# Performance work log

Hardware: AMD Instinct MI355X
Metric: run time of the kernel (lower is better)

Reference implementation:

```python
import jax, jax.numpy as jnp
import numpy as np

B, T, D, H = 2, 1024, 1024, 16
WINDOW = 32
KSZ = 2 * WINDOW + 1
MAXG = 32


def setup_inputs() -> dict:
    key = jax.random.key(0)
    ks = jax.random.split(key, 5)
    s = 0.02
    x = jax.random.normal(ks[0], (B, T, D), jnp.float32)
    Wq = jax.random.normal(ks[1], (D, D), jnp.float32) * s
    Wk = jax.random.normal(ks[2], (D, D), jnp.float32) * s
    Wv = jax.random.normal(ks[3], (D, D), jnp.float32) * s
    Wo = jax.random.normal(ks[4], (D, D), jnp.float32) * s
    # global tokens: one every T//MAXG positions (same for every batch row)
    global_mask = jnp.tile((jnp.arange(T) % (T // MAXG) == 0)[None, :], (B, 1))
    return {"x": x, "global_mask": global_mask, "Wq": Wq, "Wk": Wk,
            "Wv": Wv, "Wo": Wo, "maxG": MAXG}


def reference(x, global_mask, Wq, Wk, Wv, Wo, maxG):
    Bb, Tt, Dm = x.shape
    dh = Dm // H
    scale = dh ** -0.5

    def proj(W):
        return (x @ W.T).reshape(Bb, Tt, H, dh).transpose(0, 2, 1, 3)  # (B,H,T,dh)

    q, k, v = proj(Wq), proj(Wk), proj(Wv)

    # sliding windows via zero-padded gather (== F.unfold with padding=WINDOW)
    widx = jnp.arange(Tt)[:, None] + jnp.arange(KSZ)[None, :]  # index into padded axis

    def windows(t):
        tp = jnp.pad(t, ((0, 0), (0, 0), (WINDOW, WINDOW), (0, 0)))
        return tp[:, :, widx, :]  # (B,H,T,KSZ,dh)

    Kw, Vw = windows(k), windows(v)
    scores_local = jnp.einsum('bhtd,bhtwd->bhtw', q, Kw) * scale

    # pack global-token indices (stable argsort puts True positions first, in order)
    order = jnp.argsort(jnp.logical_not(global_mask), axis=1, stable=True)
    gidx = order[:, :maxG]                                   # (B,maxG)
    gvalid = jnp.take_along_axis(global_mask, gidx, axis=1)  # (B,maxG) bool
    gather_b = jax.vmap(lambda arr, i: arr[:, i, :])         # (H,T,dh),(maxG,)->(H,maxG,dh)
    Kg = gather_b(k, gidx) * gvalid[:, None, :, None]
    Vg = gather_b(v, gidx) * gvalid[:, None, :, None]

    scores_global = jnp.einsum('bhtd,bhgd->bhtg', q, Kg) * scale
    scores_global = jnp.where(gvalid[:, None, None, :], scores_global, -1e9)

    attn = jax.nn.softmax(jnp.concatenate([scores_local, scores_global], axis=-1), axis=-1)
    wl, wg = attn[..., :KSZ], attn[..., KSZ:]
    ctx = (jnp.einsum('bhtw,bhtwd->bhtd', wl, Vw)
           + jnp.einsum('bhtg,bhgd->bhtd', wg, Vg))
    out = ctx.transpose(0, 2, 1, 3).reshape(Bb, Tt, Dm) @ Wo.T

    # ---- debug full attention map (vectorized replica of the per-token loop) ----
    t = jnp.arange(Tt)
    left = jnp.maximum(0, t - WINDOW)
    win_len = jnp.minimum(Tt, t + WINDOW + 1) - left           # (T,)
    valid_w = jnp.arange(KSZ)[None, :] < win_len[:, None]      # (T,KSZ)
    s_loc = jnp.where(valid_w[None, None], scores_local, -jnp.inf)
    attn_d = jax.nn.softmax(jnp.concatenate([s_loc, scores_global], axis=-1), axis=-1)
    wl_d = attn_d[..., :KSZ] * valid_w[None, None]             # (B,H,T,KSZ)
    wg_d = attn_d[..., KSZ:] * gvalid[:, None, None, :]        # (B,H,T,maxG)
    cols = jnp.minimum(left[:, None] + jnp.arange(KSZ)[None, :], Tt - 1)  # (T,KSZ)
    rows = jnp.broadcast_to(t[:, None], (Tt, KSZ))
    full_attn = jnp.zeros((Bb, H, Tt, Tt), x.dtype)
    full_attn = full_attn.at[:, :, rows, cols].add(wl_d)
    full_attn = jax.vmap(lambda fa, w, gi: fa.at[:, :, gi].add(w))(full_attn, wg_d, gidx)
    return out, full_attn
```

## Files before the change

kernel.cpp:

```cpp
#include <hip/hip_runtime.h>

#define T_   1024
#define B_   2
#define H_   16
#define DH   64
#define D_   1024
#define WND  32
#define KSZ  65
#define NG   32

typedef float f32x4 __attribute__((ext_vector_type(4)));
typedef __bf16 bf16x8 __attribute__((ext_vector_type(8)));
typedef __bf16 bf16x4 __attribute__((ext_vector_type(4)));
typedef unsigned short u16x4 __attribute__((ext_vector_type(4)));

__device__ __forceinline__ unsigned short f2bf(float f) {
  unsigned u = __float_as_uint(f);
  return (unsigned short)((u + 0x7fffu + ((u >> 16) & 1u)) >> 16);
}

template<bool F32>
__device__ __forceinline__ bf16x8 load_cvt8(const char* p) {
  if constexpr (F32) {
    f32x4 a = *(const f32x4*)p;
    f32x4 b = *(const f32x4*)(p + 16);
    bf16x8 r;
    r[0] = (__bf16)a[0]; r[1] = (__bf16)a[1]; r[2] = (__bf16)a[2]; r[3] = (__bf16)a[3];
    r[4] = (__bf16)b[0]; r[5] = (__bf16)b[1]; r[6] = (__bf16)b[2]; r[7] = (__bf16)b[3];
    return r;
  } else {
    return *(const bf16x8*)p;
  }
}

template<int MODE, int BM, bool AF32, bool BF32>
__global__ __launch_bounds__(256) void gemm128(
    const void* __restrict__ A,
    const void* __restrict__ B0, const void* __restrict__ B1, const void* __restrict__ B2,
    void* __restrict__ C0v, void* __restrict__ C1v, void* __restrict__ C2v,
    const int* __restrict__ mask, int* __restrict__ gidxo, float* __restrict__ gvalo) {
  constexpr int K = 1024;
  constexpr int FM = BM / 32;
  constexpr int ACH = BM * 8 / 256;
  constexpr int WM = BM / 2;
  constexpr int AE = AF32 ? 4 : 2, BE = BF32 ? 4 : 2;

  if (MODE == 0 && blockIdx.x == 16) {
    if (blockIdx.y == 0 && blockIdx.z == 0 && threadIdx.x < 128) {
      int b = threadIdx.x >> 6, lane = threadIdx.x & 63;
      const int* mb = mask + b * T_;
      unsigned long long lanemask = (1ull << lane) - 1ull;
      int base = 0;
      for (int c = 0; c < 16 && base < NG; ++c) {
        int t = c * 64 + lane;
        bool m = mb[t] != 0;
        unsigned long long bal = __ballot(m);
        int rank = __popcll(bal & lanemask);
        if (m && base + rank < NG) { gidxo[b*NG+base+rank] = t; gvalo[b*NG+base+rank] = 1.f; }
        base += __popcll(bal);
      }
      if (base < NG) {
        for (int c = 0; c < 16 && base < NG; ++c) {
          int t = c * 64 + lane;
          bool m = mb[t] == 0;
          unsigned long long bal = __ballot(m);
          int rank = __popcll(bal & lanemask);
          if (m && base + rank < NG) { gidxo[b*NG+base+rank] = t; gvalo[b*NG+base+rank] = 0.f; }
          base += __popcll(bal);
        }
      }
    }
    return;
  }

  __shared__ __attribute__((aligned(16))) unsigned short SMEM[BM * 64 + 128 * 64];
  unsigned short* As = SMEM;
  unsigned short* Bs = SMEM + BM * 64;

  int m0 = blockIdx.x * BM, n0 = blockIdx.y * 128;
  int zz = (MODE == 0) ? blockIdx.z : 0;
  const char* Ab = (const char*)A;
  const char* Bb = (const char*)((MODE == 0) ? (zz == 0 ? B0 : (zz == 1 ? B1 : B2)) : B0);

  int tid = threadIdx.x;
  int w = tid >> 6, l = tid & 63;
  int wr = w >> 1, wc = w & 1;
  int lr = l & 15, kg = l >> 4;

  f32x4 acc[FM][4] = {};

  for (int kt = 0; kt < K; kt += 64) {
    __syncthreads();
#pragma unroll
    for (int i = 0; i < ACH; ++i) {
      int ci = tid + 256 * i;
      int row = ci >> 3, c8 = ci & 7;
      *(bf16x8*)&As[row * 64 + ((c8 ^ (row & 7)) * 8)] =
          load_cvt8<AF32>(Ab + ((size_t)(m0 + row) * K + kt + c8 * 8) * AE);
    }
#pragma unroll
    for (int i = 0; i < 4; ++i) {
      int ci = tid + 256 * i;
      int row = ci >> 3, c8 = ci & 7;
      *(bf16x8*)&Bs[row * 64 + ((c8 ^ (row & 7)) * 8)] =
          load_cvt8<BF32>(Bb + ((size_t)(n0 + row) * K + kt + c8 * 8) * BE);
    }
    __syncthreads();
#pragma unroll
    for (int kk = 0; kk < 2; ++kk) {
      int c8 = kk * 4 + kg;
      bf16x8 af[FM], bfr[4];
#pragma unroll
      for (int mi = 0; mi < FM; ++mi) {
        int row = wr * WM + mi * 16 + lr;
        af[mi] = *(bf16x8*)&As[row * 64 + ((c8 ^ (row & 7)) * 8)];
      }
#pragma unroll
      for (int ni = 0; ni < 4; ++ni) {
        int row = wc * 64 + ni * 16 + lr;
        bfr[ni] = *(bf16x8*)&Bs[row * 64 + ((c8 ^ (row & 7)) * 8)];
      }
#pragma unroll
      for (int mi = 0; mi < FM; ++mi)
#pragma unroll
        for (int ni = 0; ni < 4; ++ni)
          acc[mi][ni] = __builtin_amdgcn_mfma_f32_16x16x32_bf16(af[mi], bfr[ni], acc[mi][ni], 0, 0, 0);
    }
  }

  if (MODE == 1) {
    float* C = (float*)C0v;
#pragma unroll
    for (int mi = 0; mi < FM; ++mi)
#pragma unroll
      for (int ni = 0; ni < 4; ++ni) {
        int mbase = m0 + wr * WM + mi * 16 + (l >> 4) * 4;
        int n = n0 + wc * 64 + ni * 16 + lr;
#pragma unroll
        for (int r = 0; r < 4; ++r)
          C[(size_t)(mbase + r) * 1024 + n] = acc[mi][ni][r];
      }
  } else if (zz < 2) {
    unsigned short* C = (unsigned short*)(zz == 0 ? C0v : C1v);
#pragma unroll
    for (int mi = 0; mi < FM; ++mi)
#pragma unroll
      for (int ni = 0; ni < 4; ++ni) {
        int mbase = m0 + wr * WM + mi * 16 + (l >> 4) * 4;
        int n = n0 + wc * 64 + ni * 16 + lr;
#pragma unroll
        for (int r = 0; r < 4; ++r) {
          __bf16 v = (__bf16)acc[mi][ni][r];
          C[(size_t)(mbase + r) * 1024 + n] = *(unsigned short*)&v;
        }
      }
  } else {
    __syncthreads();
    char* Tb = (char*)SMEM;
#pragma unroll
    for (int mi = 0; mi < FM; ++mi)
#pragma unroll
      for (int ni = 0; ni < 4; ++ni) {
        int mb2 = wr * WM + mi * 16 + (l >> 4) * 4;
        int nl = wc * 64 + ni * 16 + lr;
        bf16x4 pk;
        pk[0] = (__bf16)acc[mi][ni][0]; pk[1] = (__bf16)acc[mi][ni][1];
        pk[2] = (__bf16)acc[mi][ni][2]; pk[3] = (__bf16)acc[mi][ni][3];
        *(bf16x4*)(Tb + ((nl * 256 + mb2 * 2) ^ ((nl & 7) << 4))) = pk;
      }
    __syncthreads();
    unsigned short* C = (unsigned short*)C2v;
    int bb = m0 >> 10, tbase = m0 & 1023;
#pragma unroll
    for (int it = 0; it < 8; ++it) {
      int ci = tid + 256 * it;
      int dl = ci >> 4, tc = ci & 15;
      bf16x8 v = *(bf16x8*)(Tb + ((dl * 256 + tc * 16) ^ ((dl & 7) << 4)));
      int n = n0 + dl, hh = n >> 6, dd = n & 63;
      *(bf16x8*)&C[((size_t)(bb * H_ + hh) * DH + dd) * T_ + tbase + tc * 8] = v;
    }
  }
}

__global__ __launch_bounds__(512, 4) void attn_kernel(
    const unsigned short* __restrict__ qg, const unsigned short* __restrict__ kg_,
    const unsigned short* __restrict__ vg,
    const int* __restrict__ gidx_g, const float* __restrict__ gval_g,
    unsigned short* __restrict__ ctxb, float* __restrict__ fa) {
  int tid = threadIdx.x;
  int t0 = blockIdx.x * 32;
  int h = blockIdx.y, b = blockIdx.z;
  int lane = tid & 63, wv = tid >> 6;

  __shared__ __attribute__((aligned(16))) unsigned short QbL[32 * 64];
  __shared__ __attribute__((aligned(16))) unsigned short KbL[128 * 64];
  __shared__ __attribute__((aligned(16))) unsigned short VtL[64 * 128];
  __shared__ __attribute__((aligned(16))) unsigned short WbL[32 * 128];
  __shared__ __attribute__((aligned(16))) float Sf[32][132];
  __shared__ float m_out_s[32], invdo_s[32], rowfac_s[32];
  __shared__ int   gidx_s[32];
  __shared__ float gval_s[32];

  if (tid < 32) { gidx_s[tid] = gidx_g[b * NG + tid]; gval_s[tid] = gval_g[b * NG + tid]; }
  ((unsigned long long*)WbL)[tid] = 0ull;
  ((unsigned long long*)WbL)[tid + 512] = 0ull;
  __syncthreads();

  const unsigned short* qbh = qg + (size_t)(b * T_ + t0) * D_ + h * DH;
  const unsigned short* kbh = kg_ + (size_t)(b * T_) * D_ + h * DH;
  const unsigned short* vbh = vg + (size_t)(b * H_ + h) * DH * T_;

  if (tid < 256) {
    int r = tid >> 3, c8 = tid & 7;
    bf16x8 v = *(const bf16x8*)(qbh + (size_t)r * D_ + c8 * 8);
    *(bf16x8*)((char*)QbL + ((r * 128 + c8 * 16) ^ ((r & 7) << 4))) = v;
  }
#pragma unroll
  for (int it = 0; it < 2; ++it) {
    int fi = tid + it * 512;
    int r = fi >> 3, c8 = fi & 7;
    int col; bool valid;
    if (r < 96) { col = t0 - 32 + r; valid = (col >= 0 && col < T_); }
    else { int g = r - 96; valid = gval_s[g] > 0.f; col = valid ? gidx_s[g] : 0; }
    bf16x8 v = {};
    if (valid) v = *(const bf16x8*)(kbh + (size_t)col * D_ + c8 * 8);
    *(bf16x8*)((char*)KbL + ((r * 128 + c8 * 16) ^ ((r & 7) << 4))) = v;
  }
#pragma unroll
  for (int it = 0; it < 2; ++it) {
    int fi = tid + it * 512;
    if (fi < 768) {
      int d = fi / 12, rc = fi % 12;
      int cb = t0 - 32 + rc * 8;
      bf16x8 v = {};
      if (cb >= 0 && cb < T_) v = *(const bf16x8*)(vbh + d * T_ + cb);
      *(bf16x8*)((char*)VtL + ((d * 256 + rc * 16) ^ ((d & 7) << 4))) = v;
    }
  }
#pragma unroll
  for (int it = 0; it < 4; ++it) {
    int fi = tid + it * 512;
    int d = fi >> 5, g = fi & 31;
    unsigned short v = 0;
    if (gval_s[g] > 0.f) v = vbh[d * T_ + gidx_s[g]];
    *(unsigned short*)((char*)VtL + ((d * 256 + (96 + g) * 2) ^ ((d & 7) << 4))) = v;
  }
  __syncthreads();

  {
    int mt = wv & 1, nq = wv >> 1;
    int lrr = lane & 15, kgl = lane >> 4;
    int arow = mt * 16 + lrr;
    f32x4 acc0 = {}, acc1 = {};
#pragma unroll
    for (int s = 0; s < 2; ++s) {
      int c = s * 4 + kgl;
      bf16x8 a = *(bf16x8*)((char*)QbL + ((arow * 128 + c * 16) ^ ((arow & 7) << 4)));
      int br0 = nq * 32 + lrr, br1 = nq * 32 + 16 + lrr;
      bf16x8 b0 = *(bf16x8*)((char*)KbL + ((br0 * 128 + c * 16) ^ ((br0 & 7) << 4)));
      bf16x8 b1 = *(bf16x8*)((char*)KbL + ((br1 * 128 + c * 16) ^ ((br1 & 7) << 4)));
      acc0 = __builtin_amdgcn_mfma_f32_16x16x32_bf16(a, b0, acc0, 0, 0, 0);
      acc1 = __builtin_amdgcn_mfma_f32_16x16x32_bf16(a, b1, acc1, 0, 0, 0);
    }
    int orow = mt * 16 + (lane >> 4) * 4;
#pragma unroll
    for (int i = 0; i < 4; ++i) {
      Sf[orow + i][nq * 32 + lrr] = acc0[i] * 0.125f;
      Sf[orow + i][nq * 32 + 16 + lrr] = acc1[i] * 0.125f;
    }
  }
  __syncthreads();

  {
    int r = tid >> 4, lg = tid & 15;
    int t_abs = t0 + r;
    int left = (t_abs - WND > 0) ? (t_abs - WND) : 0;
    int tmp = t_abs + WND + 1; if (tmp > T_) tmp = T_;
    int wl = tmp - left;
    float sv[8]; bool vld[8], vdd[8];
#pragma unroll
    for (int ii = 0; ii < 8; ++ii) {
      int c = lg + ii * 16;
      bool loc = (c >= r && c <= r + 64);
      bool glob = (c >= 96);
      float s = Sf[r][c];
      if (glob && !(gval_s[c - 96] > 0.f)) s = -1e9f;
      vld[ii] = loc || glob;
      vdd[ii] = loc ? ((c - r) < wl) : glob;
      sv[ii] = s;
    }
    float mo = -1e30f, md = -1e30f;
#pragma unroll
    for (int ii = 0; ii < 8; ++ii) {
      if (vld[ii]) mo = fmaxf(mo, sv[ii]);
      if (vdd[ii]) md = fmaxf(md, sv[ii]);
    }
#pragma unroll
    for (int o = 1; o < 16; o <<= 1) {
      mo = fmaxf(mo, __shfl_xor(mo, o, 16));
      md = fmaxf(md, __shfl_xor(md, o, 16));
    }
    float eo = 0.f, ed = 0.f;
#pragma unroll
    for (int ii = 0; ii < 8; ++ii) {
      if (vld[ii]) eo += __expf(sv[ii] - mo);
      if (vdd[ii]) ed += __expf(sv[ii] - md);
    }
#pragma unroll
    for (int o = 1; o < 16; o <<= 1) {
      eo += __shfl_xor(eo, o, 16);
      ed += __shfl_xor(ed, o, 16);
    }
    if (lg == 0) {
      m_out_s[r] = mo;
      invdo_s[r] = 1.f / eo;
      rowfac_s[r] = (eo / ed) * __expf(mo - md);
    }
  }
  __syncthreads();

  for (int idx = tid; idx < 32 * 97; idx += 512) {
    int t = idx / 97;
    int j = idx - t * 97;
    int cc = (j < KSZ) ? (t + j) : (j + 31);
    float s = Sf[t][cc];
    float wgt = __expf(s - m_out_s[t]) * invdo_s[t];
    Sf[t][cc] = wgt;
    *(unsigned short*)((char*)WbL + ((t * 256 + cc * 2) ^ ((t & 7) << 4))) = f2bf(wgt);
  }
  __syncthreads();

  {
    int mt = wv >> 1, nt = wv & 1;
    int lrr = lane & 15, kgl = lane >> 4;
    int arow = mt * 16 + lrr;
    int brow = nt * 16 + lrr;
    f32x4 acc = {};
#pragma unroll
    for (int s = 0; s < 4; ++s) {
      int c = s * 4 + kgl;
      bf16x8 a = *(bf16x8*)((char*)VtL + ((arow * 256 + c * 16) ^ ((arow & 7) << 4)));
      bf16x8 bb = *(bf16x8*)((char*)WbL + ((brow * 256 + c * 16) ^ ((brow & 7) << 4)));
      acc = __builtin_amdgcn_mfma_f32_16x16x32_bf16(a, bb, acc, 0, 0, 0);
    }
    int t = nt * 16 + lrr;
    int dbase = mt * 16 + (lane >> 4) * 4;
    u16x4 st;
    st.x = f2bf(acc[0]); st.y = f2bf(acc[1]); st.z = f2bf(acc[2]); st.w = f2bf(acc[3]);
    *(u16x4*)(ctxb + ((size_t)(b * T_ + t0 + t)) * D_ + h * DH + dbase) = st;
  }

  {
    int rp = tid >> 8;
    int c0 = (tid & 255) * 4;
    unsigned gm = 0;
#pragma unroll
    for (int g = 0; g < NG; ++g) {
      int gc = gidx_s[g];
      if (gval_s[g] > 0.f && gc >= c0 && gc < c0 + 4) gm |= (1u << g);
    }
#pragma unroll 2
    for (int rr = 0; rr < 16; ++rr) {
      int r = rr * 2 + rp;
      int t_abs = t0 + r;
      int left = (t_abs - WND > 0) ? (t_abs - WND) : 0;
      int tmp = t_abs + WND + 1; if (tmp > T_) tmp = T_;
      int wl = tmp - left;
      float rf = rowfac_s[r];
      f32x4 o = {0.f, 0.f, 0.f, 0.f};
      int jj0 = c0 - left;
      if (jj0 > -4 && jj0 < wl) {
#pragma unroll
        for (int e = 0; e < 4; ++e) {
          int jj = jj0 + e;
          if (jj >= 0 && jj < wl) o[e] = Sf[r][r + jj] * rf;
        }
      }
      if (gm) {
        unsigned mm = gm;
        while (mm) {
          int g = __ffs(mm) - 1; mm &= mm - 1;
          int e = gidx_s[g] - c0;
          o[e] += Sf[r][96 + g] * rf;
        }
      }
      float* dst = fa + (((size_t)(b * H_ + h) * T_) + t_abs) * T_ + c0;
      *(f32x4*)dst = o;
    }
  }
}

extern "C" void kernel_launch(void* const* d_in, const int* in_sizes, int n_in,
                              void* d_out, int out_size, void* d_ws, size_t ws_size,
                              hipStream_t stream) {
  const float* x   = (const float*)d_in[0];
  const int* gmask = (const int*)d_in[1];
  const float* wq  = (const float*)d_in[2];
  const float* wk  = (const float*)d_in[3];
  const float* wv  = (const float*)d_in[4];
  const float* wo  = (const float*)d_in[5];

  char* ws = (char*)d_ws;
  unsigned short* qb   = (unsigned short*)ws;
  unsigned short* kb   = qb + 2 * 1048576;
  unsigned short* vtb  = kb + 2 * 1048576;
  unsigned short* ctxb = vtb + 2 * 1048576;
  int*   gidx = (int*)(ctxb + 2 * 1048576);
  float* gval = (float*)(gidx + 64);

  float* outp = (float*)d_out;
  float* fa   = outp + 2097152;

  gemm128<0, 128, true, true><<<dim3(17, 8, 3), dim3(256), 0, stream>>>(
      x, wq, wk, wv, qb, kb, vtb, gmask, gidx, gval);
  attn_kernel<<<dim3(32, 16, 2), dim3(512), 0, stream>>>(qb, kb, vtb, gidx, gval, ctxb, fa);
  gemm128<1, 64, false, true><<<dim3(32, 8, 1), dim3(256), 0, stream>>>(
      ctxb, wo, wo, wo, outp, outp, outp, nullptr, nullptr, nullptr);
}
```

Baseline: 95.02 us.

## Precast inputs to bf16, use global_load_lds, move full_attn write into output GEMM

A separate conversion kernel casts x and all four weight matrices to bf16 once per call. The GEMMs can then stream tiles into LDS with direct global_load_lds. The dense full_attn map write moves out of the attention kernel. Attention now spills its weights and row factors to a workspace, and extra blocks in the output-projection GEMM scatter the 128MB map concurrently with the matmul tiles. This aims to overlap the bandwidth-bound map write with GEMM compute, at the cost of an extra conversion pass and a roughly 16MB workspace round trip.

```diff
diff --git a/kernel.cpp b/kernel.cpp
--- a/kernel.cpp
+++ b/kernel.cpp
@@ -19,34 +19,19 @@
   return (unsigned short)((u + 0x7fffu + ((u >> 16) & 1u)) >> 16);
 }
 
-template<bool F32>
-__device__ __forceinline__ bf16x8 load_cvt8(const char* p) {
-  if constexpr (F32) {
-    f32x4 a = *(const f32x4*)p;
-    f32x4 b = *(const f32x4*)(p + 16);
-    bf16x8 r;
-    r[0] = (__bf16)a[0]; r[1] = (__bf16)a[1]; r[2] = (__bf16)a[2]; r[3] = (__bf16)a[3];
-    r[4] = (__bf16)b[0]; r[5] = (__bf16)b[1]; r[6] = (__bf16)b[2]; r[7] = (__bf16)b[3];
-    return r;
-  } else {
-    return *(const bf16x8*)p;
-  }
-}
-
-template<int MODE, int BM, bool AF32, bool BF32>
-__global__ __launch_bounds__(256) void gemm128(
-    const void* __restrict__ A,
-    const void* __restrict__ B0, const void* __restrict__ B1, const void* __restrict__ B2,
-    void* __restrict__ C0v, void* __restrict__ C1v, void* __restrict__ C2v,
+__device__ __forceinline__ void gload16(const unsigned short* g, unsigned short* l) {
+  __builtin_amdgcn_global_load_lds(
+      (const __attribute__((address_space(1))) unsigned int*)g,
+      (__attribute__((address_space(3))) unsigned int*)l, 16, 0, 0);
+}
+
+__global__ __launch_bounds__(256) void cvt_kernel(const float* __restrict__ x,
+    const float* __restrict__ wq, const float* __restrict__ wk,
+    const float* __restrict__ wv, const float* __restrict__ wo,
+    unsigned short* __restrict__ dst,
     const int* __restrict__ mask, int* __restrict__ gidxo, float* __restrict__ gvalo) {
-  constexpr int K = 1024;
-  constexpr int FM = BM / 32;
-  constexpr int ACH = BM * 8 / 256;
-  constexpr int WM = BM / 2;
-  constexpr int AE = AF32 ? 4 : 2, BE = BF32 ? 4 : 2;
-
-  if (MODE == 0 && blockIdx.x == 16) {
-    if (blockIdx.y == 0 && blockIdx.z == 0 && threadIdx.x < 128) {
+  if (blockIdx.x == 6144) {
+    if (threadIdx.x < 128) {
       int b = threadIdx.x >> 6, lane = threadIdx.x & 63;
       const int* mb = mask + b * T_;
       unsigned long long lanemask = (1ull << lane) - 1ull;
@@ -72,17 +57,102 @@
     }
     return;
   }
-
+  int idx = (blockIdx.x * 256 + threadIdx.x) * 4;
+  int r = idx >> 20;
+  const float* src; int off;
+  if (r < 2)       { src = x;  off = idx; }
+  else if (r == 2) { src = wq; off = idx - 2 * 1048576; }
+  else if (r == 3) { src = wk; off = idx - 3 * 1048576; }
+  else if (r == 4) { src = wv; off = idx - 4 * 1048576; }
+  else             { src = wo; off = idx - 5 * 1048576; }
+  f32x4 v = *(const f32x4*)(src + off);
+  u16x4 o;
+  o.x = f2bf(v[0]); o.y = f2bf(v[1]); o.z = f2bf(v[2]); o.w = f2bf(v[3]);
+  *(u16x4*)(dst + idx) = o;
+}
+
+template<int MODE, int BM>
+__global__ __launch_bounds__(256) void gemm128(
+    const unsigned short* __restrict__ A,
+    const unsigned short* __restrict__ B0, const unsigned short* __restrict__ B1,
+    const unsigned short* __restrict__ B2,
+    void* __restrict__ C0v, void* __restrict__ C1v, void* __restrict__ C2v,
+    const float* __restrict__ wsum, const float* __restrict__ rfb,
+    const int* __restrict__ gidxg, const float* __restrict__ gvalg,
+    float* __restrict__ fa) {
+  constexpr int K = 1024;
+  constexpr int FM = BM / 32;
+  constexpr int ACH = BM * 8 / 256;
+  constexpr int WM = BM / 2;
   __shared__ __attribute__((aligned(16))) unsigned short SMEM[BM * 64 + 128 * 64];
+  int tid = threadIdx.x;
+
+  if (MODE == 1 && blockIdx.x >= 32) {
+    int wid = (blockIdx.x - 32) * 8 + blockIdx.y;
+    float* Ws = (float*)SMEM;
+    float* rfs = Ws + 32 * 128;
+    int* gidxs = (int*)(rfs + 32);
+    float* gvals = (float*)(gidxs + 32);
+#pragma unroll 1
+    for (int u = 0; u < 4; ++u) {
+      int unit = wid * 4 + u;
+      int b = unit >> 9, bh = unit >> 5;
+      int t0 = (unit & 31) * 32;
+      __syncthreads();
+      const float* src = wsum + (size_t)unit * 4096;
+      *(f32x4*)&Ws[tid * 4]        = *(const f32x4*)&src[tid * 4];
+      *(f32x4*)&Ws[1024 + tid * 4] = *(const f32x4*)&src[1024 + tid * 4];
+      *(f32x4*)&Ws[2048 + tid * 4] = *(const f32x4*)&src[2048 + tid * 4];
+      *(f32x4*)&Ws[3072 + tid * 4] = *(const f32x4*)&src[3072 + tid * 4];
+      if (tid < 32) {
+        rfs[tid] = rfb[unit * 32 + tid];
+        gidxs[tid] = gidxg[b * NG + tid];
+        gvals[tid] = gvalg[b * NG + tid];
+      }
+      __syncthreads();
+      int c0 = tid * 4;
+      unsigned gm = 0;
+#pragma unroll
+      for (int g = 0; g < NG; ++g) {
+        int gc = gidxs[g];
+        if (gvals[g] > 0.f && gc >= c0 && gc < c0 + 4) gm |= (1u << g);
+      }
+#pragma unroll 2
+      for (int r = 0; r < 32; ++r) {
+        int t_abs = t0 + r;
+        int left = (t_abs - WND > 0) ? (t_abs - WND) : 0;
+        int tmp = t_abs + WND + 1; if (tmp > T_) tmp = T_;
+        int wl = tmp - left;
+        float rf = rfs[r];
+        f32x4 o = {0.f, 0.f, 0.f, 0.f};
+        int jj0 = c0 - left;
+        if (jj0 > -4 && jj0 < wl) {
+#pragma unroll
+          for (int e = 0; e < 4; ++e) {
+            int jj = jj0 + e;
+            if (jj >= 0 && jj < wl) o[e] = Ws[r * 128 + r + jj] * rf;
+          }
+        }
+        if (gm) {
+          unsigned mm = gm;
+          while (mm) {
+            int g = __ffs(mm) - 1; mm &= mm - 1;
+            o[gidxs[g] - c0] += Ws[r * 128 + 96 + g] * rf;
+          }
+        }
+        *(f32x4*)(fa + ((size_t)(bh * T_) + t_abs) * T_ + c0) = o;
+      }
+    }
+    return;
+  }
+
   unsigned short* As = SMEM;
   unsigned short* Bs = SMEM + BM * 64;
-
   int m0 = blockIdx.x * BM, n0 = blockIdx.y * 128;
   int zz = (MODE == 0) ? blockIdx.z : 0;
-  const char* Ab = (const char*)A;
-  const char* Bb = (const char*)((MODE == 0) ? (zz == 0 ? B0 : (zz == 1 ? B1 : B2)) : B0);
-
-  int tid = threadIdx.x;
+  const unsigned short* Ab = A;
+  const unsigned short* Bb = (MODE == 0) ? (zz == 0 ? B0 : (zz == 1 ? B1 : B2)) : B0;
+
   int w = tid >> 6, l = tid & 63;
   int wr = w >> 1, wc = w & 1;
   int lr = l & 15, kg = l >> 4;
@@ -94,16 +164,14 @@
 #pragma unroll
     for (int i = 0; i < ACH; ++i) {
       int ci = tid + 256 * i;
-      int row = ci >> 3, c8 = ci & 7;
-      *(bf16x8*)&As[row * 64 + ((c8 ^ (row & 7)) * 8)] =
-          load_cvt8<AF32>(Ab + ((size_t)(m0 + row) * K + kt + c8 * 8) * AE);
+      int row = ci >> 3, c8 = (ci & 7) ^ (row & 7);
+      gload16(Ab + (size_t)(m0 + row) * K + kt + c8 * 8, As + ci * 8);
     }
 #pragma unroll
     for (int i = 0; i < 4; ++i) {
       int ci = tid + 256 * i;
-      int row = ci >> 3, c8 = ci & 7;
-      *(bf16x8*)&Bs[row * 64 + ((c8 ^ (row & 7)) * 8)] =
-          load_cvt8<BF32>(Bb + ((size_t)(n0 + row) * K + kt + c8 * 8) * BE);
+      int row = ci >> 3, c8 = (ci & 7) ^ (row & 7);
+      gload16(Bb + (size_t)(n0 + row) * K + kt + c8 * 8, Bs + ci * 8);
     }
     __syncthreads();
 #pragma unroll
@@ -186,7 +254,7 @@
     const unsigned short* __restrict__ qg, const unsigned short* __restrict__ kg_,
     const unsigned short* __restrict__ vg,
     const int* __restrict__ gidx_g, const float* __restrict__ gval_g,
-    unsigned short* __restrict__ ctxb, float* __restrict__ fa) {
+    unsigned short* __restrict__ ctxb, float* __restrict__ wsum, float* __restrict__ rfb) {
   int tid = threadIdx.x;
   int t0 = blockIdx.x * 32;
   int h = blockIdx.y, b = blockIdx.z;
@@ -331,6 +399,18 @@
   __syncthreads();
 
   {
+    int unit = (b * H_ + h) * 32 + blockIdx.x;
+    float* dstw = wsum + (size_t)unit * 4096;
+#pragma unroll
+    for (int it = 0; it < 2; ++it) {
+      int idx = tid + it * 512;
+      int r = idx >> 5, c4 = (idx & 31) * 4;
+      *(f32x4*)&dstw[r * 128 + c4] = *(const f32x4*)&Sf[r][c4];
+    }
+    if (tid < 32) rfb[unit * 32 + tid] = rowfac_s[tid];
+  }
+
+  {
     int mt = wv >> 1, nt = wv & 1;
     int lrr = lane & 15, kgl = lane >> 4;
     int arow = mt * 16 + lrr;
@@ -348,45 +428,6 @@
     u16x4 st;
     st.x = f2bf(acc[0]); st.y = f2bf(acc[1]); st.z = f2bf(acc[2]); st.w = f2bf(acc[3]);
     *(u16x4*)(ctxb + ((size_t)(b * T_ + t0 + t)) * D_ + h * DH + dbase) = st;
-  }
-
-  {
-    int rp = tid >> 8;
-    int c0 = (tid & 255) * 4;
-    unsigned gm = 0;
-#pragma unroll
-    for (int g = 0; g < NG; ++g) {
-      int gc = gidx_s[g];
-      if (gval_s[g] > 0.f && gc >= c0 && gc < c0 + 4) gm |= (1u << g);
-    }
-#pragma unroll 2
-    for (int rr = 0; rr < 16; ++rr) {
-      int r = rr * 2 + rp;
-      int t_abs = t0 + r;
-      int left = (t_abs - WND > 0) ? (t_abs - WND) : 0;
-      int tmp = t_abs + WND + 1; if (tmp > T_) tmp = T_;
-      int wl = tmp - left;
-      float rf = rowfac_s[r];
-      f32x4 o = {0.f, 0.f, 0.f, 0.f};
-      int jj0 = c0 - left;
-      if (jj0 > -4 && jj0 < wl) {
-#pragma unroll
-        for (int e = 0; e < 4; ++e) {
-          int jj = jj0 + e;
-          if (jj >= 0 && jj < wl) o[e] = Sf[r][r + jj] * rf;
-        }
-      }
-      if (gm) {
-        unsigned mm = gm;
-        while (mm) {
-          int g = __ffs(mm) - 1; mm &= mm - 1;
-          int e = gidx_s[g] - c0;
-          o[e] += Sf[r][96 + g] * rf;
-        }
-      }
-      float* dst = fa + (((size_t)(b * H_ + h) * T_) + t_abs) * T_ + c0;
-      *(f32x4*)dst = o;
-    }
   }
 }
 
@@ -400,20 +441,28 @@
   const float* wv  = (const float*)d_in[4];
   const float* wo  = (const float*)d_in[5];
 
-  char* ws = (char*)d_ws;
-  unsigned short* qb   = (unsigned short*)ws;
-  unsigned short* kb   = qb + 2 * 1048576;
-  unsigned short* vtb  = kb + 2 * 1048576;
-  unsigned short* ctxb = vtb + 2 * 1048576;
-  int*   gidx = (int*)(ctxb + 2 * 1048576);
+  unsigned short* arena = (unsigned short*)d_ws;
+  unsigned short* xb  = arena;
+  unsigned short* wqb = arena + 2 * 1048576;
+  unsigned short* wkb = arena + 3 * 1048576;
+  unsigned short* wvb = arena + 4 * 1048576;
+  unsigned short* wob = arena + 5 * 1048576;
+  unsigned short* qb   = arena + 6 * 1048576;
+  unsigned short* kb   = arena + 8 * 1048576;
+  unsigned short* vtb  = arena + 10 * 1048576;
+  unsigned short* ctxb = arena + 12 * 1048576;
+  float* wsum = (float*)(arena + 14 * 1048576);
+  float* rfb  = wsum + 1024 * 4096;
+  int*   gidx = (int*)(rfb + 32768);
   float* gval = (float*)(gidx + 64);
 
   float* outp = (float*)d_out;
   float* fa   = outp + 2097152;
 
-  gemm128<0, 128, true, true><<<dim3(17, 8, 3), dim3(256), 0, stream>>>(
-      x, wq, wk, wv, qb, kb, vtb, gmask, gidx, gval);
-  attn_kernel<<<dim3(32, 16, 2), dim3(512), 0, stream>>>(qb, kb, vtb, gidx, gval, ctxb, fa);
-  gemm128<1, 64, false, true><<<dim3(32, 8, 1), dim3(256), 0, stream>>>(
-      ctxb, wo, wo, wo, outp, outp, outp, nullptr, nullptr, nullptr);
-}
+  cvt_kernel<<<dim3(6145), dim3(256), 0, stream>>>(x, wq, wk, wv, wo, xb, gmask, gidx, gval);
+  gemm128<0, 128><<<dim3(16, 8, 3), dim3(256), 0, stream>>>(
+      xb, wqb, wkb, wvb, qb, kb, vtb, nullptr, nullptr, nullptr, nullptr, nullptr);
+  attn_kernel<<<dim3(32, 16, 2), dim3(512), 0, stream>>>(qb, kb, vtb, gidx, gval, ctxb, wsum, rfb);
+  gemm128<1, 64><<<dim3(64, 8, 1), dim3(256), 0, stream>>>(
+      ctxb, wob, wob, wob, outp, outp, outp, wsum, rfb, gidx, gval, fa);
+}
```

Result: slower. 117.1 us (+23.2%).

## Pre-convert inputs and weights to bf16 in a separate kernel before GEMMs

Applied to the files above, without the earlier changes.

Adds a conversion kernel that turns x and all four weight matrices from fp32 to bf16 in a workspace, and also does the global-index packing there. The GEMMs then load bf16 directly instead of converting fp32 on every tile load, which halves their load bytes and removes repeated conversion work. The QKV GEMM tile shrinks from BM=128 to 64, giving 768 blocks instead of 384, and the transposed V store is generalized for that tile size. The cost is an extra launch plus a full fp32 read and bf16 write pass over about 24 MB of inputs.

```diff
diff --git a/kernel.cpp b/kernel.cpp
--- a/kernel.cpp
+++ b/kernel.cpp
@@ -19,34 +19,13 @@
   return (unsigned short)((u + 0x7fffu + ((u >> 16) & 1u)) >> 16);
 }
 
-template<bool F32>
-__device__ __forceinline__ bf16x8 load_cvt8(const char* p) {
-  if constexpr (F32) {
-    f32x4 a = *(const f32x4*)p;
-    f32x4 b = *(const f32x4*)(p + 16);
-    bf16x8 r;
-    r[0] = (__bf16)a[0]; r[1] = (__bf16)a[1]; r[2] = (__bf16)a[2]; r[3] = (__bf16)a[3];
-    r[4] = (__bf16)b[0]; r[5] = (__bf16)b[1]; r[6] = (__bf16)b[2]; r[7] = (__bf16)b[3];
-    return r;
-  } else {
-    return *(const bf16x8*)p;
-  }
-}
-
-template<int MODE, int BM, bool AF32, bool BF32>
-__global__ __launch_bounds__(256) void gemm128(
-    const void* __restrict__ A,
-    const void* __restrict__ B0, const void* __restrict__ B1, const void* __restrict__ B2,
-    void* __restrict__ C0v, void* __restrict__ C1v, void* __restrict__ C2v,
+__global__ __launch_bounds__(256) void cvt_kernel(const float* __restrict__ x,
+    const float* __restrict__ wq, const float* __restrict__ wk,
+    const float* __restrict__ wv, const float* __restrict__ wo,
+    unsigned short* __restrict__ dst,
     const int* __restrict__ mask, int* __restrict__ gidxo, float* __restrict__ gvalo) {
-  constexpr int K = 1024;
-  constexpr int FM = BM / 32;
-  constexpr int ACH = BM * 8 / 256;
-  constexpr int WM = BM / 2;
-  constexpr int AE = AF32 ? 4 : 2, BE = BF32 ? 4 : 2;
-
-  if (MODE == 0 && blockIdx.x == 16) {
-    if (blockIdx.y == 0 && blockIdx.z == 0 && threadIdx.x < 128) {
+  if (blockIdx.x == 6144) {
+    if (threadIdx.x < 128) {
       int b = threadIdx.x >> 6, lane = threadIdx.x & 63;
       const int* mb = mask + b * T_;
       unsigned long long lanemask = (1ull << lane) - 1ull;
@@ -72,15 +51,36 @@
     }
     return;
   }
-
+  int idx = (blockIdx.x * 256 + threadIdx.x) * 4;
+  int r = idx >> 20;
+  const float* src; int off;
+  if (r < 2)       { src = x;  off = idx; }
+  else if (r == 2) { src = wq; off = idx - 2 * 1048576; }
+  else if (r == 3) { src = wk; off = idx - 3 * 1048576; }
+  else if (r == 4) { src = wv; off = idx - 4 * 1048576; }
+  else             { src = wo; off = idx - 5 * 1048576; }
+  f32x4 v = *(const f32x4*)(src + off);
+  u16x4 o;
+  o.x = f2bf(v[0]); o.y = f2bf(v[1]); o.z = f2bf(v[2]); o.w = f2bf(v[3]);
+  *(u16x4*)(dst + idx) = o;
+}
+
+template<int MODE, int BM>
+__global__ __launch_bounds__(256) void gemm128(const unsigned short* __restrict__ A,
+    const unsigned short* __restrict__ B0, const unsigned short* __restrict__ B1,
+    const unsigned short* __restrict__ B2,
+    void* __restrict__ C0v, void* __restrict__ C1v, void* __restrict__ C2v) {
+  constexpr int K = 1024;
+  constexpr int FM = BM / 32;
+  constexpr int ACH = BM * 8 / 256;
+  constexpr int WM = BM / 2;
   __shared__ __attribute__((aligned(16))) unsigned short SMEM[BM * 64 + 128 * 64];
   unsigned short* As = SMEM;
   unsigned short* Bs = SMEM + BM * 64;
 
   int m0 = blockIdx.x * BM, n0 = blockIdx.y * 128;
   int zz = (MODE == 0) ? blockIdx.z : 0;
-  const char* Ab = (const char*)A;
-  const char* Bb = (const char*)((MODE == 0) ? (zz == 0 ? B0 : (zz == 1 ? B1 : B2)) : B0);
+  const unsigned short* Bb = (MODE == 0) ? (zz == 0 ? B0 : (zz == 1 ? B1 : B2)) : B0;
 
   int tid = threadIdx.x;
   int w = tid >> 6, l = tid & 63;
@@ -96,14 +96,14 @@
       int ci = tid + 256 * i;
       int row = ci >> 3, c8 = ci & 7;
       *(bf16x8*)&As[row * 64 + ((c8 ^ (row & 7)) * 8)] =
-          load_cvt8<AF32>(Ab + ((size_t)(m0 + row) * K + kt + c8 * 8) * AE);
+          *(const bf16x8*)&A[(size_t)(m0 + row) * K + kt + c8 * 8];
     }
 #pragma unroll
     for (int i = 0; i < 4; ++i) {
       int ci = tid + 256 * i;
       int row = ci >> 3, c8 = ci & 7;
       *(bf16x8*)&Bs[row * 64 + ((c8 ^ (row & 7)) * 8)] =
-          load_cvt8<BF32>(Bb + ((size_t)(n0 + row) * K + kt + c8 * 8) * BE);
+          *(const bf16x8*)&Bb[(size_t)(n0 + row) * K + kt + c8 * 8];
     }
     __syncthreads();
 #pragma unroll
@@ -155,6 +155,9 @@
         }
       }
   } else {
+    constexpr int RS = BM * 2;
+    constexpr int TCH = BM / 8;
+    constexpr int NIT = 128 * TCH / 256;
     __syncthreads();
     char* Tb = (char*)SMEM;
 #pragma unroll
@@ -166,16 +169,16 @@
         bf16x4 pk;
         pk[0] = (__bf16)acc[mi][ni][0]; pk[1] = (__bf16)acc[mi][ni][1];
         pk[2] = (__bf16)acc[mi][ni][2]; pk[3] = (__bf16)acc[mi][ni][3];
-        *(bf16x4*)(Tb + ((nl * 256 + mb2 * 2) ^ ((nl & 7) << 4))) = pk;
+        *(bf16x4*)(Tb + ((nl * RS + mb2 * 2) ^ ((nl & 7) << 4))) = pk;
       }
     __syncthreads();
     unsigned short* C = (unsigned short*)C2v;
     int bb = m0 >> 10, tbase = m0 & 1023;
 #pragma unroll
-    for (int it = 0; it < 8; ++it) {
+    for (int it = 0; it < NIT; ++it) {
       int ci = tid + 256 * it;
-      int dl = ci >> 4, tc = ci & 15;
-      bf16x8 v = *(bf16x8*)(Tb + ((dl * 256 + tc * 16) ^ ((dl & 7) << 4)));
+      int dl = ci / TCH, tc = ci % TCH;
+      bf16x8 v = *(bf16x8*)(Tb + ((dl * RS + tc * 16) ^ ((dl & 7) << 4)));
       int n = n0 + dl, hh = n >> 6, dd = n & 63;
       *(bf16x8*)&C[((size_t)(bb * H_ + hh) * DH + dd) * T_ + tbase + tc * 8] = v;
     }
@@ -380,8 +383,7 @@
         unsigned mm = gm;
         while (mm) {
           int g = __ffs(mm) - 1; mm &= mm - 1;
-          int e = gidx_s[g] - c0;
-          o[e] += Sf[r][96 + g] * rf;
+          o[gidx_s[g] - c0] += Sf[r][96 + g] * rf;
         }
       }
       float* dst = fa + (((size_t)(b * H_ + h) * T_) + t_abs) * T_ + c0;
@@ -400,20 +402,24 @@
   const float* wv  = (const float*)d_in[4];
   const float* wo  = (const float*)d_in[5];
 
-  char* ws = (char*)d_ws;
-  unsigned short* qb   = (unsigned short*)ws;
-  unsigned short* kb   = qb + 2 * 1048576;
-  unsigned short* vtb  = kb + 2 * 1048576;
-  unsigned short* ctxb = vtb + 2 * 1048576;
-  int*   gidx = (int*)(ctxb + 2 * 1048576);
+  unsigned short* arena = (unsigned short*)d_ws;
+  unsigned short* xb  = arena;
+  unsigned short* wqb = arena + 2 * 1048576;
+  unsigned short* wkb = arena + 3 * 1048576;
+  unsigned short* wvb = arena + 4 * 1048576;
+  unsigned short* wob = arena + 5 * 1048576;
+  unsigned short* qb   = arena + 6 * 1048576;
+  unsigned short* kb   = arena + 8 * 1048576;
+  unsigned short* vtb  = arena + 10 * 1048576;
+  unsigned short* ctxb = arena + 12 * 1048576;
+  int*   gidx = (int*)(arena + 14 * 1048576);
   float* gval = (float*)(gidx + 64);
 
   float* outp = (float*)d_out;
   float* fa   = outp + 2097152;
 
-  gemm128<0, 128, true, true><<<dim3(17, 8, 3), dim3(256), 0, stream>>>(
-      x, wq, wk, wv, qb, kb, vtb, gmask, gidx, gval);
+  cvt_kernel<<<dim3(6145), dim3(256), 0, stream>>>(x, wq, wk, wv, wo, xb, gmask, gidx, gval);
+  gemm128<0, 64><<<dim3(32, 8, 3), dim3(256), 0, stream>>>(xb, wqb, wkb, wvb, qb, kb, vtb);
   attn_kernel<<<dim3(32, 16, 2), dim3(512), 0, stream>>>(qb, kb, vtb, gidx, gval, ctxb, fa);
-  gemm128<1, 64, false, true><<<dim3(32, 8, 1), dim3(256), 0, stream>>>(
-      ctxb, wo, wo, wo, outp, outp, outp, nullptr, nullptr, nullptr);
+  gemm128<1, 64><<<dim3(32, 8, 1), dim3(256), 0, stream>>>(ctxb, wob, wob, wob, outp, outp, outp);
 }
```

After: 93.10 us. 2.0% less time.
